# Optimization experiments

Hardware: AMD Instinct MI355X
Metric: run time of the kernel (lower is better)

## Reference

```python
import jax, jax.numpy as jnp
import numpy as np

N_NODES = 50000
N_EDGES = 800000


def _norm(deg):
    # DGL: norm = deg^-0.5 with inf (zero-degree) replaced by 0
    return jnp.where(deg > 0, jax.lax.rsqrt(jnp.maximum(deg, 1.0)), 0.0)


def setup_inputs() -> dict:
    key = jax.random.key(0)
    ks = jax.random.split(key, 8)
    x = jax.random.normal(ks[0], (N_NODES, 128), dtype=jnp.float32)
    W1 = jax.random.normal(ks[1], (128, 128), dtype=jnp.float32) * (1.0 / np.sqrt(128))
    b1 = jnp.zeros((128,), dtype=jnp.float32)
    W2 = jax.random.normal(ks[2], (128, 8), dtype=jnp.float32) * (1.0 / np.sqrt(128))
    b2 = jnp.zeros((8,), dtype=jnp.float32)
    src = jax.random.randint(ks[3], (N_EDGES,), 0, N_NODES, dtype=jnp.int32)
    dst = jax.random.randint(ks[4], (N_EDGES,), 0, N_NODES, dtype=jnp.int32)
    graph_ids = jnp.sort(jax.random.randint(ks[5], (N_NODES,), 0, 100, dtype=jnp.int32))
    return {"x": x, "W1": W1, "b1": b1, "W2": W2, "b2": b2,
            "src": src, "dst": dst, "graph_ids": graph_ids, "num_graphs": 100}


def _graph_conv(x, W, b, src, dst, norm_src, norm_dst):
    # GraphConv norm='both': out = D_in^{-1/2} A (D_out^{-1/2} x W) + b
    h = x @ W                                   # [N, F_out]
    msg = h[src] * norm_src[src, None]          # gather + src norm, [E, F_out]
    agg = jax.ops.segment_sum(msg, dst, num_segments=x.shape[0])  # scatter-add
    return agg * norm_dst[:, None] + b


def reference(x, W1, b1, W2, b2, src, dst, graph_ids, num_graphs):
    n = x.shape[0]
    ones_e = jnp.ones((src.shape[0],), dtype=x.dtype)
    deg_out = jax.ops.segment_sum(ones_e, src, num_segments=n)
    deg_in = jax.ops.segment_sum(ones_e, dst, num_segments=n)
    norm_src = _norm(deg_out)
    norm_dst = _norm(deg_in)

    h = _graph_conv(x, W1, b1, src, dst, norm_src, norm_dst)
    h = jax.nn.relu(h)
    h = _graph_conv(h, W2, b2, src, dst, norm_src, norm_dst)

    # dgl.mean_nodes: per-graph mean of node features
    counts = jax.ops.segment_sum(jnp.ones((n,), dtype=x.dtype), graph_ids,
                                 num_segments=num_graphs)
    sums = jax.ops.segment_sum(h, graph_ids, num_segments=num_graphs)
    return sums / jnp.maximum(counts, 1.0)[:, None]
```

## Files before the change

### kernel.cpp

```cpp
#include <hip/hip_runtime.h>

#define F1 128
#define F2 8
#define CAP 64
#define RH 8192
#define ECH 16384
#define BK 32

typedef unsigned short us8 __attribute__((ext_vector_type(8)));

__device__ inline unsigned short f2bf(float f) {
  unsigned u = __float_as_uint(f);
  u += 0x7FFF + ((u >> 16) & 1);
  return (unsigned short)(u >> 16);
}
__device__ inline float bf2f(unsigned short h) {
  return __uint_as_float(((unsigned)h) << 16);
}

__global__ __launch_bounds__(256) void k_hist(const int* __restrict__ src,
                                              const int* __restrict__ dst,
                                              unsigned short* __restrict__ src16,
                                              unsigned short* __restrict__ dst16,
                                              int* __restrict__ partialA,
                                              int* __restrict__ partialB,
                                              int Epad, int E, int N) {
  __shared__ int binsA[RH];
  __shared__ int binsB[RH];
  int range0 = blockIdx.x * RH;
  int c = blockIdx.y;
  int t = threadIdx.x;
  bool writer = (blockIdx.x == 0);
  for (int i = t; i < RH; i += 256) { binsA[i] = 0; binsB[i] = 0; }
  __syncthreads();
  int e0 = c * ECH, e1 = min(e0 + ECH, Epad);
  for (int base = e0 + t * 4; base < e1; base += 1024) {
    int4 a, b;
    if (base + 4 <= E) {
      a = *(const int4*)&src[base];
      b = *(const int4*)&dst[base];
    } else {
      a.x = (base + 0 < E) ? src[base + 0] : -1;
      a.y = (base + 1 < E) ? src[base + 1] : -1;
      a.z = (base + 2 < E) ? src[base + 2] : -1;
      a.w = (base + 3 < E) ? src[base + 3] : -1;
      b.x = (base + 0 < E) ? dst[base + 0] : -1;
      b.y = (base + 1 < E) ? dst[base + 1] : -1;
      b.z = (base + 2 < E) ? dst[base + 2] : -1;
      b.w = (base + 3 < E) ? dst[base + 3] : -1;
    }
    int av[4] = {a.x, a.y, a.z, a.w};
    int bv[4] = {b.x, b.y, b.z, b.w};
#pragma unroll
    for (int j = 0; j < 4; ++j) {
      int sn = av[j] - range0;
      if (av[j] >= 0 && (unsigned)sn < (unsigned)RH) atomicAdd(&binsA[sn], 1);
      int dn = bv[j] - range0;
      if (bv[j] >= 0 && (unsigned)dn < (unsigned)RH) atomicAdd(&binsB[dn], 1);
    }
    if (writer) {
      ushort4 sa, sb;
      sa.x = av[0] >= 0 ? (unsigned short)av[0] : 0xFFFF;
      sa.y = av[1] >= 0 ? (unsigned short)av[1] : 0xFFFF;
      sa.z = av[2] >= 0 ? (unsigned short)av[2] : 0xFFFF;
      sa.w = av[3] >= 0 ? (unsigned short)av[3] : 0xFFFF;
      sb.x = bv[0] >= 0 ? (unsigned short)bv[0] : 0xFFFF;
      sb.y = bv[1] >= 0 ? (unsigned short)bv[1] : 0xFFFF;
      sb.z = bv[2] >= 0 ? (unsigned short)bv[2] : 0xFFFF;
      sb.w = bv[3] >= 0 ? (unsigned short)bv[3] : 0xFFFF;
      *(ushort4*)&src16[base] = sa;
      *(ushort4*)&dst16[base] = sb;
    }
  }
  __syncthreads();
  for (int i = t; i < RH; i += 256) {
    int n = range0 + i;
    if (n < N) {
      partialA[c * N + n] = binsA[i];
      partialB[c * N + n] = binsB[i];
    }
  }
}

__global__ void k_starts(const int* __restrict__ partialA, const int* __restrict__ partialB,
                         int* __restrict__ starts, int* __restrict__ cnt,
                         float* __restrict__ norm_src, float* __restrict__ norm_dst,
                         unsigned short* __restrict__ esrc16,
                         unsigned short* __restrict__ h1n,
                         float* __restrict__ h2n,
                         float* __restrict__ gsum,
                         int N, int NCH, int NGF) {
  int n = blockIdx.x * 256 + threadIdx.x;
  if (n < NGF) gsum[n] = 0.f;
  if (n < 16) {
    us8 z = {0, 0, 0, 0, 0, 0, 0, 0};
    *(us8*)&h1n[(size_t)N * 128 + n * 8] = z;
  }
  if (n < 8) h2n[(size_t)N * 8 + n] = 0.f;
  if (n < N) {
    int dout = 0;
#pragma unroll 8
    for (int c = 0; c < NCH; ++c) dout += partialA[c * N + n];
    int run = n * CAP;
#pragma unroll 8
    for (int c = 0; c < NCH; ++c) {
      starts[c * N + n] = run;
      run += partialB[c * N + n];
    }
    int din = run - n * CAP;
    int cn = min(din, CAP);
    cnt[n] = cn;
    int cp = (cn + 15) & ~15;
    for (int pos = cn; pos < cp; ++pos) esrc16[n * CAP + pos] = (unsigned short)N;
    norm_src[n] = dout > 0 ? rsqrtf((float)dout) : 0.f;
    norm_dst[n] = din > 0 ? rsqrtf((float)din) : 0.f;
  }
}

__global__ __launch_bounds__(256) void k_scatter(const unsigned short* __restrict__ src16,
                                                 const unsigned short* __restrict__ dst16,
                                                 const int* __restrict__ starts,
                                                 unsigned short* __restrict__ esrc16,
                                                 int Epad, int N) {
  __shared__ int cur[RH];
  int range0 = blockIdx.x * RH;
  int c = blockIdx.y;
  int t = threadIdx.x;
  for (int i = t; i < RH; i += 256) {
    int n = range0 + i;
    cur[i] = (n < N) ? starts[c * N + n] : 0;
  }
  __syncthreads();
  int e0 = c * ECH, e1 = min(e0 + ECH, Epad);
  for (int base = e0 + t * 8; base < e1; base += 2048) {
    us8 a = *(const us8*)&src16[base];
    us8 b = *(const us8*)&dst16[base];
#pragma unroll
    for (int j = 0; j < 8; ++j) {
      int dn = (int)b[j] - range0;
      if ((unsigned)dn < (unsigned)RH) {
        int node = range0 + dn;
        int p = atomicAdd(&cur[dn], 1);
        if (p < (node + 1) * CAP) esrc16[p] = a[j];
      }
    }
  }
}

__global__ __launch_bounds__(256) void k_gemm1(const float* __restrict__ x,
                                               const float* __restrict__ W1,
                                               const float* __restrict__ norm_src,
                                               unsigned short* __restrict__ h1n, int N) {
  __shared__ float xsT[BK][132];
  __shared__ float Wl[BK][132];
  int row0 = blockIdx.x * 128;
  int tid = threadIdx.x;
  int tc = tid & 15;
  int tr = tid >> 4;
  float acc[8][8] = {{0.f}};

  for (int kb = 0; kb < 128; kb += BK) {
    __syncthreads();
#pragma unroll
    for (int it = 0; it < 4; ++it) {
      int i = tid + it * 256;
      int r = i >> 3, kq = i & 7;
      int grow = row0 + r;
      float4 v = make_float4(0.f, 0.f, 0.f, 0.f);
      if (grow < N) v = *(const float4*)&x[(size_t)grow * 128 + kb + kq * 4];
      xsT[kq * 4 + 0][r] = v.x;
      xsT[kq * 4 + 1][r] = v.y;
      xsT[kq * 4 + 2][r] = v.z;
      xsT[kq * 4 + 3][r] = v.w;
    }
#pragma unroll
    for (int it = 0; it < 4; ++it) {
      int i = tid + it * 256;
      int k = i >> 5, c4 = i & 31;
      *(float4*)&Wl[k][c4 * 4] = *(const float4*)&W1[(size_t)(kb + k) * 128 + c4 * 4];
    }
    __syncthreads();
#pragma unroll 2
    for (int k = 0; k < BK; ++k) {
      float4 xa = *(float4*)&xsT[k][tr * 8];
      float4 xb = *(float4*)&xsT[k][tr * 8 + 4];
      float4 wa = *(float4*)&Wl[k][tc * 8];
      float4 wb = *(float4*)&Wl[k][tc * 8 + 4];
      float xs[8] = {xa.x, xa.y, xa.z, xa.w, xb.x, xb.y, xb.z, xb.w};
      float ws[8] = {wa.x, wa.y, wa.z, wa.w, wb.x, wb.y, wb.z, wb.w};
#pragma unroll
      for (int i = 0; i < 8; ++i)
#pragma unroll
        for (int j = 0; j < 8; ++j) acc[i][j] += xs[i] * ws[j];
    }
  }
#pragma unroll
  for (int i = 0; i < 8; ++i) {
    int grow = row0 + tr * 8 + i;
    if (grow < N) {
      float ns = norm_src[grow];
      us8 o;
#pragma unroll
      for (int j = 0; j < 8; ++j) o[j] = f2bf(acc[i][j] * ns);
      *(us8*)&h1n[(size_t)grow * 128 + tc * 8] = o;
    }
  }
}

__global__ __launch_bounds__(256) void k_agg1f(const unsigned short* __restrict__ h1n,
                                               const int* __restrict__ cnt,
                                               const unsigned short* __restrict__ esrc16,
                                               const float* __restrict__ norm_dst,
                                               const float* __restrict__ norm_src,
                                               const float* __restrict__ b1,
                                               const float* __restrict__ W2,
                                               float* __restrict__ h2n, int N) {
  int tid = threadIdx.x;
  int lane = tid & 63;
  int g = lane >> 4;
  int fl = lane & 15;
  int node = (blockIdx.x * 256 + tid - lane) / 16 + g;
  if (node >= N) return;
  int nb = (cnt[node] + 15) >> 4;
  size_t i0 = (size_t)node * CAP;
  ushort4 myss = *(const ushort4*)&esrc16[i0 + fl * 4];
  unsigned u0 = (unsigned)myss.x | ((unsigned)myss.y << 16);
  unsigned u1 = (unsigned)myss.z | ((unsigned)myss.w << 16);
  int gbase = g << 4;
  float acc[8] = {0.f, 0.f, 0.f, 0.f, 0.f, 0.f, 0.f, 0.f};
  for (int b = 0; b < nb; ++b) {
#pragma unroll
    for (int t4 = 0; t4 < 16; t4 += 4) {
      int owner = gbase + (b << 2) + (t4 >> 2);
      unsigned w0 = __shfl(u0, owner);
      unsigned w1 = __shfl(u1, owner);
      int s0 = w0 & 0xffff, s1 = w0 >> 16;
      int s2 = w1 & 0xffff, s3 = w1 >> 16;
      us8 v0 = *(const us8*)&h1n[(size_t)s0 * 128 + fl * 8];
      us8 v1 = *(const us8*)&h1n[(size_t)s1 * 128 + fl * 8];
      us8 v2 = *(const us8*)&h1n[(size_t)s2 * 128 + fl * 8];
      us8 v3 = *(const us8*)&h1n[(size_t)s3 * 128 + fl * 8];
#pragma unroll
      for (int j = 0; j < 8; ++j)
        acc[j] += (bf2f(v0[j]) + bf2f(v1[j])) + (bf2f(v2[j]) + bf2f(v3[j]));
    }
  }
  float nd = norm_dst[node];
  float4 bb0 = *(const float4*)&b1[fl * 8];
  float4 bb1 = *(const float4*)&b1[fl * 8 + 4];
  float r[8];
  r[0] = fmaxf(acc[0] * nd + bb0.x, 0.f);
  r[1] = fmaxf(acc[1] * nd + bb0.y, 0.f);
  r[2] = fmaxf(acc[2] * nd + bb0.z, 0.f);
  r[3] = fmaxf(acc[3] * nd + bb0.w, 0.f);
  r[4] = fmaxf(acc[4] * nd + bb1.x, 0.f);
  r[5] = fmaxf(acc[5] * nd + bb1.y, 0.f);
  r[6] = fmaxf(acc[6] * nd + bb1.z, 0.f);
  r[7] = fmaxf(acc[7] * nd + bb1.w, 0.f);
  float4 pa = make_float4(0.f, 0.f, 0.f, 0.f);
  float4 pb = make_float4(0.f, 0.f, 0.f, 0.f);
#pragma unroll
  for (int jj = 0; jj < 8; ++jj) {
    float4 wa = *(const float4*)&W2[(fl * 8 + jj) * 8];
    float4 wb = *(const float4*)&W2[(fl * 8 + jj) * 8 + 4];
    pa.x += r[jj] * wa.x; pa.y += r[jj] * wa.y;
    pa.z += r[jj] * wa.z; pa.w += r[jj] * wa.w;
    pb.x += r[jj] * wb.x; pb.y += r[jj] * wb.y;
    pb.z += r[jj] * wb.z; pb.w += r[jj] * wb.w;
  }
#pragma unroll
  for (int d = 8; d >= 1; d >>= 1) {
    pa.x += __shfl_down(pa.x, d); pa.y += __shfl_down(pa.y, d);
    pa.z += __shfl_down(pa.z, d); pa.w += __shfl_down(pa.w, d);
    pb.x += __shfl_down(pb.x, d); pb.y += __shfl_down(pb.y, d);
    pb.z += __shfl_down(pb.z, d); pb.w += __shfl_down(pb.w, d);
  }
  if (fl == 0) {
    float ns = norm_src[node];
    pa.x *= ns; pa.y *= ns; pa.z *= ns; pa.w *= ns;
    pb.x *= ns; pb.y *= ns; pb.z *= ns; pb.w *= ns;
    *(float4*)&h2n[(size_t)node * 8] = pa;
    *(float4*)&h2n[(size_t)node * 8 + 4] = pb;
  }
}

__global__ __launch_bounds__(256) void k_agg2pool(const float* __restrict__ h2n,
                                                  const int* __restrict__ cnt,
                                                  const unsigned short* __restrict__ esrc16,
                                                  const float* __restrict__ norm_dst,
                                                  const float* __restrict__ b2,
                                                  const int* __restrict__ gids,
                                                  float* __restrict__ gsum, int N) {
  __shared__ float bins[16 * 8];
  __shared__ int sg0;
  int tid = threadIdx.x;
  if (tid < 128) bins[tid] = 0.f;
  int base = blockIdx.x * 32;
  if (tid == 0) sg0 = gids[min(base, N - 1)];
  __syncthreads();
  int node = base + (tid >> 3);
  int j = tid & 7;
  if (node < N) {
    int cp = (cnt[node] + 15) & ~15;
    int i0 = node * CAP;
    float acc = 0.f;
    for (int i = 0; i < cp; i += 4) {
      ushort4 ss = *(const ushort4*)&esrc16[i0 + i];
      acc += (h2n[(size_t)ss.x * 8 + j] + h2n[(size_t)ss.y * 8 + j]) +
             (h2n[(size_t)ss.z * 8 + j] + h2n[(size_t)ss.w * 8 + j]);
    }
    float r = acc * norm_dst[node] + b2[j];
    int delta = gids[node] - sg0;
    if (delta < 16) atomicAdd(&bins[delta * 8 + j], r);
    else atomicAdd(&gsum[gids[node] * 8 + j], r);
  }
  __syncthreads();
  if (tid < 128) {
    float v = bins[tid];
    if (v != 0.f) atomicAdd(&gsum[(sg0 + (tid >> 3)) * 8 + (tid & 7)], v);
  }
}

__global__ void k_final(const float* __restrict__ gsum, const int* __restrict__ gids,
                        float* __restrict__ out, int NG, int N) {
  int i = blockIdx.x * 256 + threadIdx.x;
  if (i < NG * F2) {
    int g = i >> 3;
    int lo = 0, hi = N;
    while (lo < hi) { int m = (lo + hi) >> 1; if (gids[m] < g) lo = m + 1; else hi = m; }
    int lb = lo;
    lo = 0; hi = N;
    while (lo < hi) { int m = (lo + hi) >> 1; if (gids[m] <= g) lo = m + 1; else hi = m; }
    int cnt = lo - lb;
    out[i] = gsum[i] / fmaxf((float)cnt, 1.f);
  }
}

extern "C" void kernel_launch(void* const* d_in, const int* in_sizes, int n_in,
                              void* d_out, int out_size, void* d_ws, size_t ws_size,
                              hipStream_t stream) {
  const float* x  = (const float*)d_in[0];
  const float* W1 = (const float*)d_in[1];
  const float* b1 = (const float*)d_in[2];
  const float* W2 = (const float*)d_in[3];
  const float* b2 = (const float*)d_in[4];
  const int* src  = (const int*)d_in[5];
  const int* dst  = (const int*)d_in[6];
  const int* gids = (const int*)d_in[7];
  int N = in_sizes[0] / F1;
  int E = in_sizes[5];
  int NG = out_size / F2;
  float* out = (float*)d_out;

  int Epad = (E + 2047) & ~2047;
  int NR  = (N + RH - 1) / RH;
  int NCH = (Epad + ECH - 1) / ECH;

  char* p = (char*)d_ws;
  auto alloc = [&](size_t bytes) -> void* {
    void* r = (void*)p;
    p += (bytes + 255) & ~(size_t)255;
    return r;
  };
  float* gsum    = (float*)alloc((size_t)NG * F2 * 4);
  unsigned short* src16 = (unsigned short*)alloc((size_t)Epad * 2);
  unsigned short* dst16 = (unsigned short*)alloc((size_t)Epad * 2);
  int* cnt       = (int*)alloc((size_t)N * 4);
  float* norm_src = (float*)alloc((size_t)N * 4);
  float* norm_dst = (float*)alloc((size_t)N * 4);
  unsigned short* esrc16 = (unsigned short*)alloc((size_t)N * CAP * 2);
  unsigned short* h1n = (unsigned short*)alloc((size_t)(N + 1) * F1 * 2);
  float* h2n     = (float*)alloc((size_t)(N + 1) * F2 * 4);
  int* partialA  = (int*)alloc((size_t)NCH * N * 4);
  int* partialB  = (int*)alloc((size_t)NCH * N * 4);
  int* starts    = (int*)alloc((size_t)NCH * N * 4);
  (void)ws_size; (void)n_in;

  k_hist<<<dim3(NR, NCH), 256, 0, stream>>>(src, dst, src16, dst16,
                                            partialA, partialB, Epad, E, N);
  k_starts<<<(N + 255) / 256, 256, 0, stream>>>(partialA, partialB, starts, cnt,
                                                norm_src, norm_dst, esrc16, h1n, h2n,
                                                gsum, N, NCH, NG * F2);
  k_scatter<<<dim3(NR, NCH), 256, 0, stream>>>(src16, dst16, starts, esrc16, Epad, N);
  k_gemm1<<<(N + 127) / 128, 256, 0, stream>>>(x, W1, norm_src, h1n, N);
  k_agg1f<<<(N + 15) / 16, 256, 0, stream>>>(h1n, cnt, esrc16, norm_dst, norm_src, b1, W2, h2n, N);
  k_agg2pool<<<((N * 8 + 255) / 256), 256, 0, stream>>>(h2n, cnt, esrc16, norm_dst, b2, gids, gsum, N);
  k_final<<<(NG * F2 + 255) / 256, 256, 0, stream>>>(gsum, gids, out, NG, N);
}
```

Measured before the change: 227.2 us.

## Merge scatter with GEMM1 and fold final pooling into last block

```diff
diff --git a/kernel.cpp b/kernel.cpp
--- a/kernel.cpp
+++ b/kernel.cpp
@@ -89,8 +89,10 @@
                          unsigned short* __restrict__ h1n,
                          float* __restrict__ h2n,
                          float* __restrict__ gsum,
+                         int* __restrict__ done,
                          int N, int NCH, int NGF) {
   int n = blockIdx.x * 256 + threadIdx.x;
+  if (n == 0) *done = 0;
   if (n < NGF) gsum[n] = 0.f;
   if (n < 16) {
     us8 z = {0, 0, 0, 0, 0, 0, 0, 0};
@@ -117,92 +119,96 @@
   }
 }
 
-__global__ __launch_bounds__(256) void k_scatter(const unsigned short* __restrict__ src16,
-                                                 const unsigned short* __restrict__ dst16,
-                                                 const int* __restrict__ starts,
-                                                 unsigned short* __restrict__ esrc16,
-                                                 int Epad, int N) {
-  __shared__ int cur[RH];
-  int range0 = blockIdx.x * RH;
-  int c = blockIdx.y;
-  int t = threadIdx.x;
-  for (int i = t; i < RH; i += 256) {
-    int n = range0 + i;
-    cur[i] = (n < N) ? starts[c * N + n] : 0;
-  }
-  __syncthreads();
-  int e0 = c * ECH, e1 = min(e0 + ECH, Epad);
-  for (int base = e0 + t * 8; base < e1; base += 2048) {
-    us8 a = *(const us8*)&src16[base];
-    us8 b = *(const us8*)&dst16[base];
-#pragma unroll
-    for (int j = 0; j < 8; ++j) {
-      int dn = (int)b[j] - range0;
-      if ((unsigned)dn < (unsigned)RH) {
-        int node = range0 + dn;
-        int p = atomicAdd(&cur[dn], 1);
-        if (p < (node + 1) * CAP) esrc16[p] = a[j];
-      }
-    }
-  }
-}
-
-__global__ __launch_bounds__(256) void k_gemm1(const float* __restrict__ x,
-                                               const float* __restrict__ W1,
-                                               const float* __restrict__ norm_src,
-                                               unsigned short* __restrict__ h1n, int N) {
-  __shared__ float xsT[BK][132];
-  __shared__ float Wl[BK][132];
-  int row0 = blockIdx.x * 128;
+struct SMemU {
+  union {
+    int cur[RH];
+    struct { float xsT[BK][132]; float Wl[BK][132]; } g;
+  } u;
+};
+
+__global__ __launch_bounds__(256) void k_scatgemm(const unsigned short* __restrict__ src16,
+                                                  const unsigned short* __restrict__ dst16,
+                                                  const int* __restrict__ starts,
+                                                  unsigned short* __restrict__ esrc16,
+                                                  const float* __restrict__ x,
+                                                  const float* __restrict__ W1,
+                                                  const float* __restrict__ norm_src,
+                                                  unsigned short* __restrict__ h1n,
+                                                  int Epad, int N, int NCH, int NRNCH) {
+  __shared__ SMemU sm;
   int tid = threadIdx.x;
-  int tc = tid & 15;
-  int tr = tid >> 4;
-  float acc[8][8] = {{0.f}};
-
-  for (int kb = 0; kb < 128; kb += BK) {
+  if ((int)blockIdx.x < NRNCH) {
+    int range0 = ((int)blockIdx.x / NCH) * RH;
+    int c = (int)blockIdx.x % NCH;
+    for (int i = tid; i < RH; i += 256) {
+      int n = range0 + i;
+      sm.u.cur[i] = (n < N) ? starts[c * N + n] : 0;
+    }
     __syncthreads();
-#pragma unroll
-    for (int it = 0; it < 4; ++it) {
-      int i = tid + it * 256;
-      int r = i >> 3, kq = i & 7;
-      int grow = row0 + r;
-      float4 v = make_float4(0.f, 0.f, 0.f, 0.f);
-      if (grow < N) v = *(const float4*)&x[(size_t)grow * 128 + kb + kq * 4];
-      xsT[kq * 4 + 0][r] = v.x;
-      xsT[kq * 4 + 1][r] = v.y;
-      xsT[kq * 4 + 2][r] = v.z;
-      xsT[kq * 4 + 3][r] = v.w;
-    }
-#pragma unroll
-    for (int it = 0; it < 4; ++it) {
-      int i = tid + it * 256;
-      int k = i >> 5, c4 = i & 31;
-      *(float4*)&Wl[k][c4 * 4] = *(const float4*)&W1[(size_t)(kb + k) * 128 + c4 * 4];
-    }
-    __syncthreads();
+    int e0 = c * ECH, e1 = min(e0 + ECH, Epad);
+    for (int base = e0 + tid * 8; base < e1; base += 2048) {
+      us8 a = *(const us8*)&src16[base];
+      us8 b = *(const us8*)&dst16[base];
+#pragma unroll
+      for (int j = 0; j < 8; ++j) {
+        int dn = (int)b[j] - range0;
+        if ((unsigned)dn < (unsigned)RH) {
+          int node = range0 + dn;
+          int p = atomicAdd(&sm.u.cur[dn], 1);
+          if (p < (node + 1) * CAP) esrc16[p] = a[j];
+        }
+      }
+    }
+  } else {
+    int row0 = ((int)blockIdx.x - NRNCH) * 128;
+    int tc = tid & 15;
+    int tr = tid >> 4;
+    float acc[8][8] = {{0.f}};
+    for (int kb = 0; kb < 128; kb += BK) {
+      __syncthreads();
+#pragma unroll
+      for (int it = 0; it < 4; ++it) {
+        int i = tid + it * 256;
+        int r = i >> 3, kq = i & 7;
+        int grow = row0 + r;
+        float4 v = make_float4(0.f, 0.f, 0.f, 0.f);
+        if (grow < N) v = *(const float4*)&x[(size_t)grow * 128 + kb + kq * 4];
+        sm.u.g.xsT[kq * 4 + 0][r] = v.x;
+        sm.u.g.xsT[kq * 4 + 1][r] = v.y;
+        sm.u.g.xsT[kq * 4 + 2][r] = v.z;
+        sm.u.g.xsT[kq * 4 + 3][r] = v.w;
+      }
+#pragma unroll
+      for (int it = 0; it < 4; ++it) {
+        int i = tid + it * 256;
+        int k = i >> 5, c4 = i & 31;
+        *(float4*)&sm.u.g.Wl[k][c4 * 4] = *(const float4*)&W1[(size_t)(kb + k) * 128 + c4 * 4];
+      }
+      __syncthreads();
 #pragma unroll 2
-    for (int k = 0; k < BK; ++k) {
-      float4 xa = *(float4*)&xsT[k][tr * 8];
-      float4 xb = *(float4*)&xsT[k][tr * 8 + 4];
-      float4 wa = *(float4*)&Wl[k][tc * 8];
-      float4 wb = *(float4*)&Wl[k][tc * 8 + 4];
-      float xs[8] = {xa.x, xa.y, xa.z, xa.w, xb.x, xb.y, xb.z, xb.w};
-      float ws[8] = {wa.x, wa.y, wa.z, wa.w, wb.x, wb.y, wb.z, wb.w};
-#pragma unroll
-      for (int i = 0; i < 8; ++i)
-#pragma unroll
-        for (int j = 0; j < 8; ++j) acc[i][j] += xs[i] * ws[j];
-    }
-  }
-#pragma unroll
-  for (int i = 0; i < 8; ++i) {
-    int grow = row0 + tr * 8 + i;
-    if (grow < N) {
-      float ns = norm_src[grow];
-      us8 o;
-#pragma unroll
-      for (int j = 0; j < 8; ++j) o[j] = f2bf(acc[i][j] * ns);
-      *(us8*)&h1n[(size_t)grow * 128 + tc * 8] = o;
+      for (int k = 0; k < BK; ++k) {
+        float4 xa = *(float4*)&sm.u.g.xsT[k][tr * 8];
+        float4 xb = *(float4*)&sm.u.g.xsT[k][tr * 8 + 4];
+        float4 wa = *(float4*)&sm.u.g.Wl[k][tc * 8];
+        float4 wb = *(float4*)&sm.u.g.Wl[k][tc * 8 + 4];
+        float xs[8] = {xa.x, xa.y, xa.z, xa.w, xb.x, xb.y, xb.z, xb.w};
+        float ws[8] = {wa.x, wa.y, wa.z, wa.w, wb.x, wb.y, wb.z, wb.w};
+#pragma unroll
+        for (int i = 0; i < 8; ++i)
+#pragma unroll
+          for (int j = 0; j < 8; ++j) acc[i][j] += xs[i] * ws[j];
+      }
+    }
+#pragma unroll
+    for (int i = 0; i < 8; ++i) {
+      int grow = row0 + tr * 8 + i;
+      if (grow < N) {
+        float ns = norm_src[grow];
+        us8 o;
+#pragma unroll
+        for (int j = 0; j < 8; ++j) o[j] = f2bf(acc[i][j] * ns);
+        *(us8*)&h1n[(size_t)grow * 128 + tc * 8] = o;
+      }
     }
   }
 }
@@ -221,25 +227,17 @@
   int fl = lane & 15;
   int node = (blockIdx.x * 256 + tid - lane) / 16 + g;
   if (node >= N) return;
-  int nb = (cnt[node] + 15) >> 4;
-  size_t i0 = (size_t)node * CAP;
-  ushort4 myss = *(const ushort4*)&esrc16[i0 + fl * 4];
-  unsigned u0 = (unsigned)myss.x | ((unsigned)myss.y << 16);
-  unsigned u1 = (unsigned)myss.z | ((unsigned)myss.w << 16);
-  int gbase = g << 4;
+  int cp = (cnt[node] + 15) & ~15;
+  int i0 = node * CAP;
   float acc[8] = {0.f, 0.f, 0.f, 0.f, 0.f, 0.f, 0.f, 0.f};
-  for (int b = 0; b < nb; ++b) {
+  for (int i = 0; i < cp; i += 16) {
 #pragma unroll
     for (int t4 = 0; t4 < 16; t4 += 4) {
-      int owner = gbase + (b << 2) + (t4 >> 2);
-      unsigned w0 = __shfl(u0, owner);
-      unsigned w1 = __shfl(u1, owner);
-      int s0 = w0 & 0xffff, s1 = w0 >> 16;
-      int s2 = w1 & 0xffff, s3 = w1 >> 16;
-      us8 v0 = *(const us8*)&h1n[(size_t)s0 * 128 + fl * 8];
-      us8 v1 = *(const us8*)&h1n[(size_t)s1 * 128 + fl * 8];
-      us8 v2 = *(const us8*)&h1n[(size_t)s2 * 128 + fl * 8];
-      us8 v3 = *(const us8*)&h1n[(size_t)s3 * 128 + fl * 8];
+      ushort4 ss = *(const ushort4*)&esrc16[i0 + i + t4];
+      us8 v0 = *(const us8*)&h1n[(size_t)ss.x * 128 + fl * 8];
+      us8 v1 = *(const us8*)&h1n[(size_t)ss.y * 128 + fl * 8];
+      us8 v2 = *(const us8*)&h1n[(size_t)ss.z * 128 + fl * 8];
+      us8 v3 = *(const us8*)&h1n[(size_t)ss.w * 128 + fl * 8];
 #pragma unroll
       for (int j = 0; j < 8; ++j)
         acc[j] += (bf2f(v0[j]) + bf2f(v1[j])) + (bf2f(v2[j]) + bf2f(v3[j]));
@@ -290,9 +288,13 @@
                                                   const float* __restrict__ norm_dst,
                                                   const float* __restrict__ b2,
                                                   const int* __restrict__ gids,
-                                                  float* __restrict__ gsum, int N) {
+                                                  float* __restrict__ gsum,
+                                                  float* __restrict__ out,
+                                                  int* __restrict__ done,
+                                                  int NG, int N) {
   __shared__ float bins[16 * 8];
   __shared__ int sg0;
+  __shared__ bool last;
   int tid = threadIdx.x;
   if (tid < 128) bins[tid] = 0.f;
   int base = blockIdx.x * 32;
@@ -319,20 +321,25 @@
     float v = bins[tid];
     if (v != 0.f) atomicAdd(&gsum[(sg0 + (tid >> 3)) * 8 + (tid & 7)], v);
   }
-}
-
-__global__ void k_final(const float* __restrict__ gsum, const int* __restrict__ gids,
-                        float* __restrict__ out, int NG, int N) {
-  int i = blockIdx.x * 256 + threadIdx.x;
-  if (i < NG * F2) {
-    int g = i >> 3;
-    int lo = 0, hi = N;
-    while (lo < hi) { int m = (lo + hi) >> 1; if (gids[m] < g) lo = m + 1; else hi = m; }
-    int lb = lo;
-    lo = 0; hi = N;
-    while (lo < hi) { int m = (lo + hi) >> 1; if (gids[m] <= g) lo = m + 1; else hi = m; }
-    int cnt = lo - lb;
-    out[i] = gsum[i] / fmaxf((float)cnt, 1.f);
+  __syncthreads();
+  if (tid == 0) {
+    __threadfence();
+    last = (atomicAdd(done, 1) == (int)gridDim.x - 1);
+  }
+  __syncthreads();
+  if (last) {
+    __threadfence();
+    for (int i = tid; i < NG * F2; i += 256) {
+      float gv = atomicAdd(&gsum[i], 0.f);
+      int gq = i >> 3;
+      int lo = 0, hi = N;
+      while (lo < hi) { int m = (lo + hi) >> 1; if (gids[m] < gq) lo = m + 1; else hi = m; }
+      int lb = lo;
+      lo = 0; hi = N;
+      while (lo < hi) { int m = (lo + hi) >> 1; if (gids[m] <= gq) lo = m + 1; else hi = m; }
+      int cntg = lo - lb;
+      out[i] = gv / fmaxf((float)cntg, 1.f);
+    }
   }
 }
 
@@ -355,6 +362,8 @@
   int Epad = (E + 2047) & ~2047;
   int NR  = (N + RH - 1) / RH;
   int NCH = (Epad + ECH - 1) / ECH;
+  int NRNCH = NR * NCH;
+  int gemmB = (N + 127) / 128;
 
   char* p = (char*)d_ws;
   auto alloc = [&](size_t bytes) -> void* {
@@ -363,6 +372,7 @@
     return r;
   };
   float* gsum    = (float*)alloc((size_t)NG * F2 * 4);
+  int* done      = (int*)alloc(256);
   unsigned short* src16 = (unsigned short*)alloc((size_t)Epad * 2);
   unsigned short* dst16 = (unsigned short*)alloc((size_t)Epad * 2);
   int* cnt       = (int*)alloc((size_t)N * 4);
@@ -380,10 +390,10 @@
                                             partialA, partialB, Epad, E, N);
   k_starts<<<(N + 255) / 256, 256, 0, stream>>>(partialA, partialB, starts, cnt,
                                                 norm_src, norm_dst, esrc16, h1n, h2n,
-                                                gsum, N, NCH, NG * F2);
-  k_scatter<<<dim3(NR, NCH), 256, 0, stream>>>(src16, dst16, starts, esrc16, Epad, N);
-  k_gemm1<<<(N + 127) / 128, 256, 0, stream>>>(x, W1, norm_src, h1n, N);
+                                                gsum, done, N, NCH, NG * F2);
+  k_scatgemm<<<NRNCH + gemmB, 256, 0, stream>>>(src16, dst16, starts, esrc16,
+                                                x, W1, norm_src, h1n, Epad, N, NCH, NRNCH);
   k_agg1f<<<(N + 15) / 16, 256, 0, stream>>>(h1n, cnt, esrc16, norm_dst, norm_src, b1, W2, h2n, N);
-  k_agg2pool<<<((N * 8 + 255) / 256), 256, 0, stream>>>(h2n, cnt, esrc16, norm_dst, b2, gids, gsum, N);
-  k_final<<<(NG * F2 + 255) / 256, 256, 0, stream>>>(gsum, gids, out, NG, N);
-}
+  k_agg2pool<<<((N * 8 + 255) / 256), 256, 0, stream>>>(h2n, cnt, esrc16, norm_dst, b2,
+                                                        gids, gsum, out, done, NG, N);
+}
```

Result: slower. 265.7 us (+16.9%).
